# Performance work log

Hardware: AMD Instinct MI355X
Metric: run time of the kernel (lower is better)

## Reference

```python
import jax, jax.numpy as jnp
import numpy as np

# dims (see shape_source): emb_dim=256, input_size=256 -> d_model=1024
B, L = 8, 1024
QUES = 4000
EMB = 256
DM = 1024          # input_size + 768
DI = 2048          # expand * d_model
N = 16             # d_state
DTR = 64           # dt_rank = ceil(d_model/16)
K = 4              # d_conv
EPS = 1e-12


def setup_inputs() -> dict:
    key = jax.random.key(0)
    ks = jax.random.split(key, 16)
    s = 0.02
    nrm = lambda k, sh: jax.random.normal(k, sh, dtype=jnp.float32) * s
    return {
        "x": jax.random.randint(ks[0], (B, L), 0, 2 * QUES + 1),
        "q_id": jax.random.randint(ks[1], (B, L), 0, QUES),
        "emb_table": nrm(ks[2], (2 * QUES + 1, EMB)),
        "ques_cont": nrm(ks[3], (QUES, 768)),
        "ln0_g": jnp.ones((DM,), jnp.float32),
        "ln0_b": jnp.zeros((DM,), jnp.float32),
        "in_proj_w": nrm(ks[4], (2 * DI, DM)),
        "conv_w": nrm(ks[5], (DI, K)),
        "conv_b": jnp.zeros((DI,), jnp.float32),
        "x_proj_w": nrm(ks[6], (DTR + 2 * N, DI)),
        "dt_proj_w": nrm(ks[7], (DI, DTR)),
        "dt_proj_b": nrm(ks[8], (DI,)),
        "A_log": jnp.log(jax.random.uniform(ks[9], (DI, N), jnp.float32, 1.0, 16.0)),
        "D_param": jnp.ones((DI,), jnp.float32),
        "out_proj_w": nrm(ks[10], (DM, DI)),
        "ln1_g": jnp.ones((DM,), jnp.float32),
        "ln1_b": jnp.zeros((DM,), jnp.float32),
        "fc_w": nrm(ks[11], (QUES, DM)),
        "fc_b": jnp.zeros((QUES,), jnp.float32),
    }


def _ln(x, g, b):
    m = x.mean(-1, keepdims=True)
    v = ((x - m) ** 2).mean(-1, keepdims=True)
    return (x - m) / jnp.sqrt(v + EPS) * g + b


def _mamba(xm, in_proj_w, conv_w, conv_b, x_proj_w, dt_proj_w, dt_proj_b,
           A_log, D_param, out_proj_w):
    # xm: [B, L, DM]
    u_r = xm @ in_proj_w.T                           # [B, L, 2*DI]
    u, r = jnp.split(u_r, 2, axis=-1)                # each [B, L, DI]
    Lq = u.shape[1]
    # causal depthwise conv1d (padding=K-1, truncated to L)
    u_pad = jnp.pad(u, ((0, 0), (K - 1, 0), (0, 0)))
    conv = sum(u_pad[:, k:k + Lq, :] * conv_w[:, k] for k in range(K)) + conv_b
    u = jax.nn.silu(conv)
    dbl = u @ x_proj_w.T                             # [B, L, DTR+2N]
    dt, Bm, Cm = dbl[..., :DTR], dbl[..., DTR:DTR + N], dbl[..., DTR + N:]
    delta = jax.nn.softplus(dt @ dt_proj_w.T + dt_proj_b)   # [B, L, DI]
    A = -jnp.exp(A_log)                              # [DI, N]

    def step(h, ins):
        d_t, b_t, c_t, u_t = ins                     # [B,DI],[B,N],[B,N],[B,DI]
        dA = jnp.exp(d_t[:, :, None] * A)            # [B, DI, N]
        h = dA * h + d_t[:, :, None] * b_t[:, None, :] * u_t[:, :, None]
        y_t = jnp.einsum('bdn,bn->bd', h, c_t)
        return h, y_t

    xs = (delta.transpose(1, 0, 2), Bm.transpose(1, 0, 2),
          Cm.transpose(1, 0, 2), u.transpose(1, 0, 2))
    h0 = jnp.zeros((u.shape[0], DI, N), u.dtype)
    _, ys = jax.lax.scan(step, h0, xs)               # ys: [L, B, DI]
    y = ys.transpose(1, 0, 2) + u * D_param
    y = y * jax.nn.silu(r)
    return y @ out_proj_w.T                          # [B, L, DM]


def reference(x, q_id, emb_table, ques_cont, ln0_g, ln0_b, in_proj_w, conv_w,
              conv_b, x_proj_w, dt_proj_w, dt_proj_b, A_log, D_param,
              out_proj_w, ln1_g, ln1_b, fc_w, fc_b):
    x_e = emb_table[x]                               # [B, L, 256]
    x_c = ques_cont[q_id]                            # [B, L, 768]
    item = _ln(jnp.concatenate([x_e, x_c], axis=-1), ln0_g, ln0_b)
    # source loop applies every layer to item_emb; only the last layer's
    # output is used, so compute exactly that one layer (num_layers=2 branch).
    h = _mamba(item, in_proj_w, conv_w, conv_b, x_proj_w, dt_proj_w,
               dt_proj_b, A_log, D_param, out_proj_w)
    out = _ln(h + item, ln1_g, ln1_b)
    return jax.nn.sigmoid(out @ fc_w.T + fc_b)       # [B, L, QUES]
```

## Files before the change

kernel.cpp:

```cpp
#include <hip/hip_runtime.h>
#include <cstdint>
#include <cstddef>

#define L_SEQ 1024
#define BATCH 8
#define DMODEL 1024
#define DINNER 2048
#define NSTATE 16
#define DTRANK 64
#define NQ 4000
#define NROWS (BATCH * L_SEQ)
#define CH 32
#define NCH (L_SEQ / CH)

typedef float f32x4 __attribute__((ext_vector_type(4)));
typedef __bf16 bf16x8 __attribute__((ext_vector_type(8)));

#define AS1 __attribute__((address_space(1)))
#define AS3 __attribute__((address_space(3)))

__device__ __forceinline__ unsigned short f2bf(float f) {
  union { float f; unsigned int u; } c; c.f = f;
  unsigned int u = c.u;
  unsigned int r = u + 0x7fffu + ((u >> 16) & 1u);
  return (unsigned short)(r >> 16);
}

__device__ __forceinline__ float sigmoidf_(float x) { return 1.f / (1.f + expf(-x)); }

__global__ void cast_bf16_k(const float* __restrict__ src, unsigned short* __restrict__ dst, int n) {
  int i = blockIdx.x * blockDim.x + threadIdx.x;
  if (i < n) dst[i] = f2bf(src[i]);
}

__device__ __forceinline__ float blk_sum(float v, float* s) {
  #pragma unroll
  for (int o = 32; o > 0; o >>= 1) v += __shfl_down(v, o, 64);
  int w = threadIdx.x >> 6;
  if ((threadIdx.x & 63) == 0) s[w] = v;
  __syncthreads();
  float r = s[0] + s[1] + s[2] + s[3];
  __syncthreads();
  return r;
}

__global__ __launch_bounds__(256) void embed_ln0_k(
    const int* __restrict__ x, const int* __restrict__ qid,
    const float* __restrict__ emb, const float* __restrict__ qc,
    const float* __restrict__ g, const float* __restrict__ bta,
    float* __restrict__ item, unsigned short* __restrict__ item_bf)
{
  __shared__ float sbuf[4];
  int i = blockIdx.x;
  int t = threadIdx.x;
  float4 v;
  if (t < 64) v = *(const float4*)&emb[(size_t)x[i] * 256 + t * 4];
  else        v = *(const float4*)&qc[(size_t)qid[i] * 768 + t * 4 - 256];
  float tot = blk_sum(v.x + v.y + v.z + v.w, sbuf);
  float mean = tot * (1.f / 1024.f);
  float dx = v.x - mean, dy = v.y - mean, dz = v.z - mean, dw = v.w - mean;
  float var = blk_sum(dx*dx + dy*dy + dz*dz + dw*dw, sbuf) * (1.f / 1024.f);
  float rstd = rsqrtf(var + 1e-12f);
  float vals[4] = {dx, dy, dz, dw};
  size_t rb = (size_t)i * 1024;
  #pragma unroll
  for (int j = 0; j < 4; j++) {
    int c = t * 4 + j;
    float o = vals[j] * rstd * g[c] + bta[c];
    item[rb + c] = o;
    item_bf[rb + c] = f2bf(o);
  }
}

template <int EPI>
__global__ __launch_bounds__(256) void gemm_bt_k(
    const unsigned short* __restrict__ A, const unsigned short* __restrict__ Bw,
    float* __restrict__ C, const float* __restrict__ bias,
    unsigned short* __restrict__ aux,
    int M, int N, int K)
{
  __shared__ __align__(16) unsigned short As[128 * 64];
  __shared__ __align__(16) unsigned short Bs[128 * 64];
  const int tid = threadIdx.x;
  const int m0 = blockIdx.x * 128;
  const int n0 = blockIdx.y * 128;
  const int w = tid >> 6, lane = tid & 63;
  const int wrow = (w >> 1) * 64, wcol = (w & 1) * 64;
  const int quad = lane >> 4, lid = lane & 15;

  const int srow = lane >> 3;
  const int schunk = (lane & 7) ^ srow;

  const unsigned short* Abase = A + (size_t)(m0 + w * 8 + srow) * K + schunk * 8;
  const unsigned short* Bbase[4];
  #pragma unroll
  for (int i = 0; i < 4; i++) {
    int rB = n0 + w * 8 + i * 32 + srow;
    if (rB > N - 1) rB = N - 1;
    Bbase[i] = Bw + (size_t)rB * K + schunk * 8;
  }

  f32x4 acc[4][4] = {};

  for (int k0 = 0; k0 < K; k0 += 64) {
    #pragma unroll
    for (int i = 0; i < 4; i++) {
      int rA = w * 8 + i * 32;
      __builtin_amdgcn_global_load_lds(
          (const AS1 unsigned int*)(Abase + (size_t)i * 32 * K + k0),
          (AS3 unsigned int*)&As[rA * 64], 16, 0, 0);
      __builtin_amdgcn_global_load_lds(
          (const AS1 unsigned int*)(Bbase[i] + k0),
          (AS3 unsigned int*)&Bs[rA * 64], 16, 0, 0);
    }
    __syncthreads();
    #pragma unroll
    for (int kk = 0; kk < 64; kk += 32) {
      bf16x8 af[4], bfr[4];
      #pragma unroll
      for (int mi = 0; mi < 4; mi++) {
        int r = wrow + mi * 16 + lid;
        int slot = ((kk >> 3) + quad) ^ (lid & 7);
        af[mi] = *(const bf16x8*)&As[r * 64 + slot * 8];
      }
      #pragma unroll
      for (int ni = 0; ni < 4; ni++) {
        int r = wcol + ni * 16 + lid;
        int slot = ((kk >> 3) + quad) ^ (lid & 7);
        bfr[ni] = *(const bf16x8*)&Bs[r * 64 + slot * 8];
      }
      #pragma unroll
      for (int mi = 0; mi < 4; mi++)
        #pragma unroll
        for (int ni = 0; ni < 4; ni++)
          acc[mi][ni] = __builtin_amdgcn_mfma_f32_16x16x32_bf16(af[mi], bfr[ni], acc[mi][ni], 0, 0, 0);
    }
    __syncthreads();
  }

  #pragma unroll
  for (int mi = 0; mi < 4; mi++) {
    #pragma unroll
    for (int ni = 0; ni < 4; ni++) {
      int col = n0 + wcol + ni * 16 + lid;
      if (col >= N) continue;
      #pragma unroll
      for (int r = 0; r < 4; r++) {
        int row = m0 + wrow + mi * 16 + quad * 4 + r;
        float v = acc[mi][ni][r];
        if (EPI == 1) v = sigmoidf_(v + bias[col]);
        if (EPI == 2) { float xx = v + bias[col]; v = fmaxf(xx, 0.f) + log1pf(expf(-fabsf(xx))); }
        C[(size_t)row * N + col] = v;
        if (EPI == 3 && col < 64) aux[(size_t)row * 64 + col] = f2bf(v);
      }
    }
  }
}

template <int EPI>
__global__ __launch_bounds__(512, 2) void gemm256_k(
    const unsigned short* __restrict__ A, const unsigned short* __restrict__ Bw,
    float* __restrict__ C, const float* __restrict__ bias,
    int M, int N, int K)
{
  __shared__ __align__(16) unsigned short As[2][256 * 64];
  __shared__ __align__(16) unsigned short Bs[2][256 * 64];
  const int tid = threadIdx.x;

  const int gx = gridDim.x;
  const int nwg = gx * gridDim.y;
  int bid = blockIdx.y * gx + blockIdx.x;
  if ((nwg & 7) == 0) bid = (bid & 7) * (nwg >> 3) + (bid >> 3);
  const int m0 = (bid % gx) * 256;
  const int n0 = (bid / gx) * 256;

  const int w = tid >> 6, lane = tid & 63;
  const int wrow = (w >> 2) * 128;
  const int wcol = (w & 3) * 64;
  const int quad = lane >> 4, lid = lane & 15;

  const int srow = lane >> 3;
  const int schunk = (lane & 7) ^ srow;

  const unsigned short* Ab = A + (size_t)(m0 + w * 8 + srow) * K + schunk * 8;
  const unsigned short* Bb[4];
  #pragma unroll
  for (int i = 0; i < 4; i++) {
    int rB = n0 + w * 8 + i * 64 + srow;
    if (rB > N - 1) rB = N - 1;
    Bb[i] = Bw + (size_t)rB * K + schunk * 8;
  }

  f32x4 acc[8][4] = {};

  auto stage = [&](int buf, int k0) {
    #pragma unroll
    for (int i = 0; i < 4; i++) {
      int rg = (i * 64 + w * 8) * 64;
      __builtin_amdgcn_global_load_lds(
          (const AS1 unsigned int*)(Ab + (size_t)i * 64 * K + k0),
          (AS3 unsigned int*)&As[buf][rg], 16, 0, 0);
      __builtin_amdgcn_global_load_lds(
          (const AS1 unsigned int*)(Bb[i] + k0),
          (AS3 unsigned int*)&Bs[buf][rg], 16, 0, 0);
    }
  };

  const int nt = K >> 6;
  stage(0, 0);
  __syncthreads();

  for (int kt = 0; kt < nt; ++kt) {
    const int cur = kt & 1;
    if (kt + 1 < nt) stage(cur ^ 1, (kt + 1) << 6);

    bf16x8 bfr[4][2];
    #pragma unroll
    for (int ni = 0; ni < 4; ni++) {
      #pragma unroll
      for (int kk2 = 0; kk2 < 2; kk2++) {
        int r = wcol + ni * 16 + lid;
        int slot = (kk2 * 4 + quad) ^ (lid & 7);
        bfr[ni][kk2] = *(const bf16x8*)&Bs[cur][r * 64 + slot * 8];
      }
    }
    #pragma unroll
    for (int mi = 0; mi < 8; mi++) {
      bf16x8 af[2];
      #pragma unroll
      for (int kk2 = 0; kk2 < 2; kk2++) {
        int r = wrow + mi * 16 + lid;
        int slot = (kk2 * 4 + quad) ^ (lid & 7);
        af[kk2] = *(const bf16x8*)&As[cur][r * 64 + slot * 8];
      }
      #pragma unroll
      for (int ni = 0; ni < 4; ni++) {
        acc[mi][ni] = __builtin_amdgcn_mfma_f32_16x16x32_bf16(af[0], bfr[ni][0], acc[mi][ni], 0, 0, 0);
        acc[mi][ni] = __builtin_amdgcn_mfma_f32_16x16x32_bf16(af[1], bfr[ni][1], acc[mi][ni], 0, 0, 0);
      }
    }
    __syncthreads();
  }

  #pragma unroll
  for (int mi = 0; mi < 8; mi++) {
    #pragma unroll
    for (int ni = 0; ni < 4; ni++) {
      int col = n0 + wcol + ni * 16 + lid;
      if (col >= N) continue;
      #pragma unroll
      for (int r = 0; r < 4; r++) {
        int row = m0 + wrow + mi * 16 + quad * 4 + r;
        float v = acc[mi][ni][r];
        if (EPI == 1) v = sigmoidf_(v + bias[col]);
        C[(size_t)row * N + col] = v;
      }
    }
  }
}

__global__ void conv_silu_k(const float* __restrict__ u_r, const float* __restrict__ w,
                            const float* __restrict__ cb, float* __restrict__ uc,
                            unsigned short* __restrict__ uc_bf)
{
  int idx = blockIdx.x * blockDim.x + threadIdx.x;
  if (idx >= BATCH * L_SEQ * DINNER) return;
  int d = idx & (DINNER - 1);
  int l = (idx >> 11) & (L_SEQ - 1);
  int b = idx >> 21;
  float4 wv = ((const float4*)w)[d];
  size_t rb = ((size_t)b * L_SEQ + l) * (2 * DINNER) + d;
  float acc = cb[d];
  acc += wv.w * u_r[rb];
  if (l >= 1) acc += wv.z * u_r[rb - (2 * DINNER)];
  if (l >= 2) acc += wv.y * u_r[rb - 2 * (2 * DINNER)];
  if (l >= 3) acc += wv.x * u_r[rb - 3 * (2 * DINNER)];
  float s = acc * sigmoidf_(acc);
  uc[idx] = s;
  uc_bf[idx] = f2bf(s);
}

__global__ void a2_k(const float* __restrict__ Alog, float* __restrict__ a2t)
{
  int i = blockIdx.x * blockDim.x + threadIdx.x;
  if (i >= DINNER * NSTATE) return;
  int d = i >> 4, n = i & 15;
  a2t[n * DINNER + d] = -expf(Alog[i]) * 1.4426950408889634f;
}

__global__ __launch_bounds__(64) void scan1_k(
    const float* __restrict__ dlt, const float* __restrict__ uc,
    const float* __restrict__ dbl, const float* __restrict__ a2t,
    float* __restrict__ Pbuf, float* __restrict__ Qbuf)
{
  int c = blockIdx.x;
  int dg = blockIdx.y;
  int b = blockIdx.z;
  int d = dg * 64 + threadIdx.x;
  float a2[NSTATE], P[NSTATE], q[NSTATE];
  #pragma unroll
  for (int n = 0; n < NSTATE; n++) {
    a2[n] = a2t[n * DINNER + d];
    P[n] = 1.f; q[n] = 0.f;
  }
  size_t base = ((size_t)(b * L_SEQ + c * CH)) * DINNER + d;
  const float* bc = dbl + (size_t)(b * L_SEQ + c * CH) * 96 + 64;
  for (int t = 0; t < CH; t++) {
    float dl = dlt[base];
    float du = dl * uc[base];
    #pragma unroll
    for (int n = 0; n < NSTATE; n++) {
      float dA = exp2f(dl * a2[n]);
      q[n] = dA * q[n] + du * bc[n];
      P[n] *= dA;
    }
    base += DINNER;
    bc += 96;
  }
  size_t ob = ((size_t)((b * NCH + c) * NSTATE)) * DINNER + d;
  #pragma unroll
  for (int n = 0; n < NSTATE; n++) {
    Pbuf[ob + (size_t)n * DINNER] = P[n];
    Qbuf[ob + (size_t)n * DINNER] = q[n];
  }
}

__global__ void scan_carry_k(const float* __restrict__ Pbuf, float* __restrict__ Qbuf)
{
  int idx = blockIdx.x * blockDim.x + threadIdx.x;
  if (idx >= BATCH * NSTATE * DINNER) return;
  int d = idx & (DINNER - 1);
  int n = (idx >> 11) & 15;
  int b = idx >> 15;
  float h = 0.f;
  for (int c = 0; c < NCH; c++) {
    size_t o = ((size_t)((b * NCH + c) * NSTATE + n)) * DINNER + d;
    float P = Pbuf[o];
    float q = Qbuf[o];
    Qbuf[o] = h;
    h = P * h + q;
  }
}

__global__ __launch_bounds__(64) void scan2_k(
    const float* __restrict__ dlt, const float* __restrict__ uc,
    const float* __restrict__ dbl, const float* __restrict__ a2t,
    const float* __restrict__ Qbuf, const float* __restrict__ u_r,
    const float* __restrict__ Dp, unsigned short* __restrict__ ybf)
{
  int c = blockIdx.x;
  int dg = blockIdx.y;
  int b = blockIdx.z;
  int d = dg * 64 + threadIdx.x;
  float a2[NSTATE], h[NSTATE];
  size_t ob = ((size_t)((b * NCH + c) * NSTATE)) * DINNER + d;
  #pragma unroll
  for (int n = 0; n < NSTATE; n++) {
    a2[n] = a2t[n * DINNER + d];
    h[n] = Qbuf[ob + (size_t)n * DINNER];
  }
  float Dd = Dp[d];
  size_t base = ((size_t)(b * L_SEQ + c * CH)) * DINNER + d;
  const float* bc = dbl + (size_t)(b * L_SEQ + c * CH) * 96 + 64;
  const float* rp = u_r + (size_t)(b * L_SEQ + c * CH) * (2 * DINNER) + DINNER + d;
  for (int t = 0; t < CH; t++) {
    float dl = dlt[base];
    float uval = uc[base];
    float du = dl * uval;
    float yv = 0.f;
    #pragma unroll
    for (int n = 0; n < NSTATE; n++) {
      float dA = exp2f(dl * a2[n]);
      h[n] = dA * h[n] + du * bc[n];
      yv += h[n] * bc[NSTATE + n];
    }
    float rv = *rp;
    float val = (yv + uval * Dd) * (rv * sigmoidf_(rv));
    ybf[base] = f2bf(val);
    base += DINNER;
    bc += 96;
    rp += 2 * DINNER;
  }
}

__global__ __launch_bounds__(256) void ln1_k(
    const float* __restrict__ mamba, const float* __restrict__ item,
    const float* __restrict__ g, const float* __restrict__ bta,
    unsigned short* __restrict__ out_bf)
{
  __shared__ float sbuf[4];
  int i = blockIdx.x;
  int t = threadIdx.x;
  size_t rb = (size_t)i * 1024 + t * 4;
  float4 v = *(const float4*)&mamba[rb];
  float4 w4 = *(const float4*)&item[rb];
  v.x += w4.x; v.y += w4.y; v.z += w4.z; v.w += w4.w;
  float tot = blk_sum(v.x + v.y + v.z + v.w, sbuf);
  float mean = tot * (1.f / 1024.f);
  float dx = v.x - mean, dy = v.y - mean, dz = v.z - mean, dw = v.w - mean;
  float var = blk_sum(dx*dx + dy*dy + dz*dz + dw*dw, sbuf) * (1.f / 1024.f);
  float rstd = rsqrtf(var + 1e-12f);
  float vals[4] = {dx, dy, dz, dw};
  #pragma unroll
  for (int j = 0; j < 4; j++) {
    int c = t * 4 + j;
    out_bf[(size_t)i * 1024 + c] = f2bf(vals[j] * rstd * g[c] + bta[c]);
  }
}

extern "C" void kernel_launch(void* const* d_in, const int* in_sizes, int n_in,
                              void* d_out, int out_size, void* d_ws, size_t ws_size,
                              hipStream_t stream)
{
  (void)in_sizes; (void)n_in; (void)out_size; (void)ws_size;
  const int*   x     = (const int*)d_in[0];
  const int*   qid   = (const int*)d_in[1];
  const float* emb   = (const float*)d_in[2];
  const float* qc    = (const float*)d_in[3];
  const float* ln0g  = (const float*)d_in[4];
  const float* ln0b  = (const float*)d_in[5];
  const float* w_in  = (const float*)d_in[6];
  const float* convw = (const float*)d_in[7];
  const float* convb = (const float*)d_in[8];
  const float* w_x   = (const float*)d_in[9];
  const float* w_dt  = (const float*)d_in[10];
  const float* dtb   = (const float*)d_in[11];
  const float* Alog  = (const float*)d_in[12];
  const float* Dp    = (const float*)d_in[13];
  const float* w_out = (const float*)d_in[14];
  const float* ln1g  = (const float*)d_in[15];
  const float* ln1b  = (const float*)d_in[16];
  const float* w_fc  = (const float*)d_in[17];
  const float* fcb   = (const float*)d_in[18];
  float* out = (float*)d_out;

  char* base = (char*)d_ws;
  size_t off = 0;
  auto carve = [&](size_t bytes) -> char* {
    char* p = base + off;
    off = (off + bytes + 255) & ~(size_t)255;
    return p;
  };
  float* item  = (float*)carve((size_t)NROWS * 1024 * 4);
  float* u_r   = (float*)carve((size_t)NROWS * 4096 * 4);
  float* uc    = (float*)carve((size_t)NROWS * 2048 * 4);
  float* dbl   = (float*)carve((size_t)NROWS * 96 * 4);
  float* dlt   = (float*)carve((size_t)NROWS * 2048 * 4);
  float* mamba = (float*)carve((size_t)NROWS * 1024 * 4);
  unsigned short* bfbuf  = (unsigned short*)carve((size_t)NROWS * 2048 * 2);
  unsigned short* bw_in  = (unsigned short*)carve((size_t)4096 * 1024 * 2);
  unsigned short* bw_x   = (unsigned short*)carve((size_t)96 * 2048 * 2);
  unsigned short* bw_dt  = (unsigned short*)carve((size_t)2048 * 64 * 2);
  unsigned short* bw_out = (unsigned short*)carve((size_t)1024 * 2048 * 2);
  unsigned short* bw_fc  = (unsigned short*)carve((size_t)4000 * 1024 * 2);
  float* a2t   = (float*)carve((size_t)DINNER * NSTATE * 4);

  unsigned short* dt_bf = (unsigned short*)mamba;
  float* Pbuf = mamba;
  float* Qbuf = (float*)bfbuf;
  unsigned short* y_bf = (unsigned short*)mamba;
  float* mamba_out = u_r;

  auto cv = [&](const float* s, unsigned short* dst, int n) {
    cast_bf16_k<<<(n + 255) / 256, 256, 0, stream>>>(s, dst, n);
  };
  cv(w_in,  bw_in,  4096 * 1024);
  cv(w_x,   bw_x,   96 * 2048);
  cv(w_dt,  bw_dt,  2048 * 64);
  cv(w_out, bw_out, 1024 * 2048);
  cv(w_fc,  bw_fc,  4000 * 1024);
  a2_k<<<(DINNER * NSTATE + 255) / 256, 256, 0, stream>>>(Alog, a2t);

  embed_ln0_k<<<NROWS, 256, 0, stream>>>(x, qid, emb, qc, ln0g, ln0b, item, bfbuf);

  gemm256_k<0><<<dim3(32, 16), 512, 0, stream>>>(bfbuf, bw_in, u_r, nullptr, NROWS, 4096, 1024);

  conv_silu_k<<<(NROWS * DINNER) / 256, 256, 0, stream>>>(u_r, convw, convb, uc, bfbuf);

  gemm_bt_k<3><<<dim3(64, 1), 256, 0, stream>>>(bfbuf, bw_x, dbl, nullptr, dt_bf, NROWS, 96, 2048);

  gemm_bt_k<2><<<dim3(64, 16), 256, 0, stream>>>(dt_bf, bw_dt, dlt, dtb, nullptr, NROWS, 2048, 64);

  scan1_k<<<dim3(NCH, 32, BATCH), 64, 0, stream>>>(dlt, uc, dbl, a2t, Pbuf, Qbuf);
  scan_carry_k<<<(BATCH * NSTATE * DINNER) / 256, 256, 0, stream>>>(Pbuf, Qbuf);
  scan2_k<<<dim3(NCH, 32, BATCH), 64, 0, stream>>>(dlt, uc, dbl, a2t, Qbuf, u_r, Dp, y_bf);

  gemm_bt_k<0><<<dim3(64, 8), 256, 0, stream>>>(y_bf, bw_out, mamba_out, nullptr, nullptr, NROWS, 1024, 2048);

  ln1_k<<<NROWS, 256, 0, stream>>>(mamba_out, item, ln1g, ln1b, bfbuf);

  gemm256_k<1><<<dim3(32, 16), 512, 0, stream>>>(bfbuf, bw_fc, out, fcb, NROWS, 4000, 1024);
}
```

Measured before the change: 861.5 us.

## Triple-buffer GEMM with BK=32, manual vmcnt waits, and reuse for out_proj

Replaces the double-buffered 256x256 BK=64 GEMM with a templated triple-buffered kernel using BK=32 stages. It waits with explicit s_waitcnt vmcnt and s_barrier instead of __syncthreads, and raises wave priority around the MFMA block. A BN=128 variant now also serves the out_proj GEMM in place of the older gemm_bt_k. The goal is to overlap global-to-LDS loads with MFMA compute and cut barrier stalls, at the cost of more fragile hand-tuned wait counts and a changed LDS swizzle.

Measured after the change: 923.9 us. +7.2%, slower.

```diff
diff --git a/kernel.cpp b/kernel.cpp
--- a/kernel.cpp
+++ b/kernel.cpp
@@ -18,6 +18,9 @@
 
 #define AS1 __attribute__((address_space(1)))
 #define AS3 __attribute__((address_space(3)))
+
+#define VMCNT(n) asm volatile("s_waitcnt vmcnt(" #n ")" ::: "memory")
+#define SBARRIER() asm volatile("s_barrier" ::: "memory")
 
 __device__ __forceinline__ unsigned short f2bf(float f) {
   union { float f; unsigned int u; } c; c.f = f;
@@ -157,100 +160,114 @@
   }
 }
 
-template <int EPI>
-__global__ __launch_bounds__(512, 2) void gemm256_k(
+template <int BN, int EPI>
+__global__ __launch_bounds__(512, 2) void gemm_pipe_k(
     const unsigned short* __restrict__ A, const unsigned short* __restrict__ Bw,
     float* __restrict__ C, const float* __restrict__ bias,
     int M, int N, int K)
 {
-  __shared__ __align__(16) unsigned short As[2][256 * 64];
-  __shared__ __align__(16) unsigned short Bs[2][256 * 64];
+  constexpr int NB = BN / 64;
+  constexpr int BJ = (BN == 256) ? 2 : 1;
+  constexpr int NI = 2 + BJ;
+
+  __shared__ __align__(16) unsigned short As[3][256 * 32];
+  __shared__ __align__(16) unsigned short Bs[3][BN * 32];
+
   const int tid = threadIdx.x;
-
   const int gx = gridDim.x;
   const int nwg = gx * gridDim.y;
   int bid = blockIdx.y * gx + blockIdx.x;
-  if ((nwg & 7) == 0) bid = (bid & 7) * (nwg >> 3) + (bid >> 3);
+  bid = (bid & 7) * (nwg >> 3) + (bid >> 3);
   const int m0 = (bid % gx) * 256;
-  const int n0 = (bid / gx) * 256;
+  const int n0 = (bid / gx) * BN;
 
   const int w = tid >> 6, lane = tid & 63;
-  const int wrow = (w >> 2) * 128;
-  const int wcol = (w & 3) * 64;
+  const int wm = w >> 2, wn = w & 3;
   const int quad = lane >> 4, lid = lane & 15;
 
-  const int srow = lane >> 3;
-  const int schunk = (lane & 7) ^ srow;
-
-  const unsigned short* Ab = A + (size_t)(m0 + w * 8 + srow) * K + schunk * 8;
-  const unsigned short* Bb[4];
-  #pragma unroll
-  for (int i = 0; i < 4; i++) {
-    int rB = n0 + w * 8 + i * 64 + srow;
+  const int srow = lane >> 2;
+  const int sch  = ((lane & 3) ^ ((lane >> 3) & 3)) * 8;
+
+  const unsigned short* Ag[2];
+  int AsegE[2];
+  #pragma unroll
+  for (int j = 0; j < 2; j++) {
+    Ag[j] = A + (size_t)(m0 + 32 * w + 16 * j + srow) * K + sch;
+    AsegE[j] = (w * 2 + j) * 512;
+  }
+  const unsigned short* Bg[BJ];
+  int BsegE[BJ];
+  #pragma unroll
+  for (int j = 0; j < BJ; j++) {
+    int rB = n0 + (BN == 256 ? 32 * w + 16 * j : 16 * w) + srow;
     if (rB > N - 1) rB = N - 1;
-    Bb[i] = Bw + (size_t)rB * K + schunk * 8;
-  }
-
-  f32x4 acc[8][4] = {};
-
-  auto stage = [&](int buf, int k0) {
-    #pragma unroll
-    for (int i = 0; i < 4; i++) {
-      int rg = (i * 64 + w * 8) * 64;
+    Bg[j] = Bw + (size_t)rB * K + sch;
+    BsegE[j] = (BN == 256 ? (w * 2 + j) : w) * 512;
+  }
+
+  auto stage = [&](int buf, int t) {
+    const int ko = t * 32;
+    #pragma unroll
+    for (int j = 0; j < 2; j++)
       __builtin_amdgcn_global_load_lds(
-          (const AS1 unsigned int*)(Ab + (size_t)i * 64 * K + k0),
-          (AS3 unsigned int*)&As[buf][rg], 16, 0, 0);
+          (const AS1 unsigned int*)(Ag[j] + ko),
+          (AS3 unsigned int*)&As[buf][AsegE[j]], 16, 0, 0);
+    #pragma unroll
+    for (int j = 0; j < BJ; j++)
       __builtin_amdgcn_global_load_lds(
-          (const AS1 unsigned int*)(Bb[i] + k0),
-          (AS3 unsigned int*)&Bs[buf][rg], 16, 0, 0);
-    }
+          (const AS1 unsigned int*)(Bg[j] + ko),
+          (AS3 unsigned int*)&Bs[buf][BsegE[j]], 16, 0, 0);
   };
 
-  const int nt = K >> 6;
+  const int slot8 = (quad ^ ((lid >> 1) & 3)) * 8;
+  const int aoff = (wm * 128 + lid) * 32 + slot8;
+  const int boff = (wn * (BN / 4) + lid) * 32 + slot8;
+
+  f32x4 acc[8][NB] = {};
+  const int nt = K >> 5;
+
   stage(0, 0);
-  __syncthreads();
-
-  for (int kt = 0; kt < nt; ++kt) {
-    const int cur = kt & 1;
-    if (kt + 1 < nt) stage(cur ^ 1, (kt + 1) << 6);
-
-    bf16x8 bfr[4][2];
-    #pragma unroll
-    for (int ni = 0; ni < 4; ni++) {
+  stage(1, 1);
+  if constexpr (NI == 4) VMCNT(4); else VMCNT(3);
+  SBARRIER();
+
+  int bR = 0, bS = 2;
+  for (int t = 0; t < nt; ++t) {
+    const bool more = (t + 2 < nt);
+    if (more) stage(bS, t + 2);
+    __builtin_amdgcn_sched_barrier(0);
+
+    bf16x8 af[8], bfr[NB];
+    #pragma unroll
+    for (int ni = 0; ni < NB; ni++) bfr[ni] = *(const bf16x8*)&Bs[bR][boff + ni * 512];
+    #pragma unroll
+    for (int mi = 0; mi < 8; mi++)  af[mi]  = *(const bf16x8*)&As[bR][aoff + mi * 512];
+
+    __builtin_amdgcn_s_setprio(1);
+    #pragma unroll
+    for (int mi = 0; mi < 8; mi++)
       #pragma unroll
-      for (int kk2 = 0; kk2 < 2; kk2++) {
-        int r = wcol + ni * 16 + lid;
-        int slot = (kk2 * 4 + quad) ^ (lid & 7);
-        bfr[ni][kk2] = *(const bf16x8*)&Bs[cur][r * 64 + slot * 8];
-      }
-    }
-    #pragma unroll
-    for (int mi = 0; mi < 8; mi++) {
-      bf16x8 af[2];
-      #pragma unroll
-      for (int kk2 = 0; kk2 < 2; kk2++) {
-        int r = wrow + mi * 16 + lid;
-        int slot = (kk2 * 4 + quad) ^ (lid & 7);
-        af[kk2] = *(const bf16x8*)&As[cur][r * 64 + slot * 8];
-      }
-      #pragma unroll
-      for (int ni = 0; ni < 4; ni++) {
-        acc[mi][ni] = __builtin_amdgcn_mfma_f32_16x16x32_bf16(af[0], bfr[ni][0], acc[mi][ni], 0, 0, 0);
-        acc[mi][ni] = __builtin_amdgcn_mfma_f32_16x16x32_bf16(af[1], bfr[ni][1], acc[mi][ni], 0, 0, 0);
-      }
-    }
-    __syncthreads();
+      for (int ni = 0; ni < NB; ni++)
+        acc[mi][ni] = __builtin_amdgcn_mfma_f32_16x16x32_bf16(af[mi], bfr[ni], acc[mi][ni], 0, 0, 0);
+    __builtin_amdgcn_s_setprio(0);
+
+    __builtin_amdgcn_sched_barrier(0);
+    if (more) { if constexpr (NI == 4) VMCNT(4); else VMCNT(3); }
+    else VMCNT(0);
+    SBARRIER();
+    bR = (bR + 1 == 3) ? 0 : bR + 1;
+    bS = (bS + 1 == 3) ? 0 : bS + 1;
   }
 
   #pragma unroll
   for (int mi = 0; mi < 8; mi++) {
     #pragma unroll
-    for (int ni = 0; ni < 4; ni++) {
-      int col = n0 + wcol + ni * 16 + lid;
+    for (int ni = 0; ni < NB; ni++) {
+      int col = n0 + wn * (BN / 4) + ni * 16 + lid;
       if (col >= N) continue;
       #pragma unroll
       for (int r = 0; r < 4; r++) {
-        int row = m0 + wrow + mi * 16 + quad * 4 + r;
+        int row = m0 + wm * 128 + mi * 16 + quad * 4 + r;
         float v = acc[mi][ni][r];
         if (EPI == 1) v = sigmoidf_(v + bias[col]);
         C[(size_t)row * N + col] = v;
@@ -473,7 +490,7 @@
 
   embed_ln0_k<<<NROWS, 256, 0, stream>>>(x, qid, emb, qc, ln0g, ln0b, item, bfbuf);
 
-  gemm256_k<0><<<dim3(32, 16), 512, 0, stream>>>(bfbuf, bw_in, u_r, nullptr, NROWS, 4096, 1024);
+  gemm_pipe_k<256, 0><<<dim3(32, 16), 512, 0, stream>>>(bfbuf, bw_in, u_r, nullptr, NROWS, 4096, 1024);
 
   conv_silu_k<<<(NROWS * DINNER) / 256, 256, 0, stream>>>(u_r, convw, convb, uc, bfbuf);
 
@@ -485,9 +502,9 @@
   scan_carry_k<<<(BATCH * NSTATE * DINNER) / 256, 256, 0, stream>>>(Pbuf, Qbuf);
   scan2_k<<<dim3(NCH, 32, BATCH), 64, 0, stream>>>(dlt, uc, dbl, a2t, Qbuf, u_r, Dp, y_bf);
 
-  gemm_bt_k<0><<<dim3(64, 8), 256, 0, stream>>>(y_bf, bw_out, mamba_out, nullptr, nullptr, NROWS, 1024, 2048);
+  gemm_pipe_k<128, 0><<<dim3(32, 8), 512, 0, stream>>>(y_bf, bw_out, mamba_out, nullptr, NROWS, 1024, 2048);
 
   ln1_k<<<NROWS, 256, 0, stream>>>(mamba_out, item, ln1g, ln1b, bfbuf);
 
-  gemm256_k<1><<<dim3(32, 16), 512, 0, stream>>>(bfbuf, bw_fc, out, fcb, NROWS, 4000, 1024);
-}
+  gemm_pipe_k<256, 1><<<dim3(32, 16), 512, 0, stream>>>(bfbuf, bw_fc, out, fcb, NROWS, 4000, 1024);
+}
```
